# Kernel optimization log

Measured on AMD Instinct MI355X. Metric: run time of the kernel, lower is better.

Reference implementation:

```python
import jax, jax.numpy as jnp
import numpy as np

D = 2048
N_DRUG, N_PROT = 10000, 20000
E = 100000


def setup_inputs() -> dict:
    key = jax.random.key(0)
    ks = jax.random.split(key, 10)
    return {
        "x_drug": jax.random.normal(ks[0], (N_DRUG, D), dtype=jnp.float32),
        "x_protein": jax.random.normal(ks[1], (N_PROT, D), dtype=jnp.float32),
        "rel_ddi": jax.random.normal(ks[2], (D,), dtype=jnp.float32),
        "rel_dpi": jax.random.normal(ks[3], (D,), dtype=jnp.float32),
        "ddi_src": jax.random.randint(ks[4], (E,), 0, N_DRUG, dtype=jnp.int64 if jax.config.jax_enable_x64 else jnp.int32),
        "ddi_dst": jax.random.randint(ks[5], (E,), 0, N_DRUG, dtype=jnp.int64 if jax.config.jax_enable_x64 else jnp.int32),
        "dpi_src": jax.random.randint(ks[6], (E,), 0, N_DRUG, dtype=jnp.int64 if jax.config.jax_enable_x64 else jnp.int32),
        "dpi_dst": jax.random.randint(ks[7], (E,), 0, N_PROT, dtype=jnp.int64 if jax.config.jax_enable_x64 else jnp.int32),
        "ppi_src": jax.random.randint(ks[8], (E,), 0, N_PROT, dtype=jnp.int64 if jax.config.jax_enable_x64 else jnp.int32),
        "ppi_dst": jax.random.randint(ks[9], (E,), 0, N_PROT, dtype=jnp.int64 if jax.config.jax_enable_x64 else jnp.int32),
    }


def _edge_score(x_src, x_dst, src, dst, rel):
    # gather [E, D] head/tail, DistMult-style multiply-reduce, clamp to [0, 1]
    head = x_src[src]
    tail = x_dst[dst]
    score = jnp.sum(head * rel * tail, axis=-1)
    return jnp.clip(score, 0.0, 1.0)


def reference(x_drug, x_protein, rel_ddi, rel_dpi,
              ddi_src, ddi_dst, dpi_src, dpi_dst, ppi_src, ppi_dst):
    score_ddi = _edge_score(x_drug, x_drug, ddi_src, ddi_dst, rel_ddi)
    score_dpi = _edge_score(x_drug, x_protein, dpi_src, dpi_dst, rel_dpi)
    # NOTE: original module (faithfully) applies the DPI relation to PPI edges
    score_ppi = _edge_score(x_protein, x_protein, ppi_src, ppi_dst, rel_dpi)
    return (score_ddi, score_dpi, score_ppi)
```

## Files before the change

kernel.cpp:

```cpp
#include <hip/hip_runtime.h>
#include <hip/hip_fp16.h>

#define D4 512
#define T4 256
#define K_EDGES 16

__global__ __launch_bounds__(256) void cvt16(
    const float4* __restrict__ xd, const float4* __restrict__ xp,
    __half* __restrict__ drug16, __half* __restrict__ prot16,
    int nd4, int np4)
{
    int i = blockIdx.x * blockDim.x + threadIdx.x;
    const int total = nd4 + np4;
    for (; i < total; i += gridDim.x * blockDim.x) {
        float4 v; __half* o; int idx;
        if (i < nd4) { v = xd[i]; o = drug16; idx = i; }
        else         { v = xp[i - nd4]; o = prot16; idx = i - nd4; }
        __half2 h01 = __floats2half2_rn(v.x, v.y);
        __half2 h23 = __floats2half2_rn(v.z, v.w);
        uint2 pk = make_uint2(*(const unsigned*)&h01, *(const unsigned*)&h23);
        ((uint2*)o)[idx] = pk;
    }
}

__global__ void zero_ints(int* __restrict__ p, int n) {
    int i = blockIdx.x * blockDim.x + threadIdx.x;
    if (i < n) p[i] = 0;
}

__global__ void hist3(const int* __restrict__ s0, const int* __restrict__ s1,
                      const int* __restrict__ s2, int E,
                      int* __restrict__ cnt, int ndp) {
    int i = blockIdx.x * blockDim.x + threadIdx.x;
    const int total = 3 * E;
    for (; i < total; i += gridDim.x * blockDim.x) {
        if (i < E)           atomicAdd(&cnt[s0[i]], 1);
        else if (i < 2 * E)  atomicAdd(&cnt[ndp + s1[i - E]], 1);
        else                 atomicAdd(&cnt[2 * ndp + s2[i - 2 * E]], 1);
    }
}

__global__ void alloc3(const int* __restrict__ cnt, int* __restrict__ base,
                       int* __restrict__ cursors, int ndp, int CB) {
    int i = blockIdx.x * blockDim.x + threadIdx.x;
    if (i >= CB) return;
    const int lane = threadIdx.x & 63;
    const int g = (i < ndp) ? 0 : (i < 2 * ndp) ? 1 : 2;
    int c = cnt[i];
    int x = c;
#pragma unroll
    for (int d = 1; d < 64; d <<= 1) {
        int y = __shfl_up(x, d, 64);
        if (lane >= d) x += y;
    }
    int tot = __shfl(x, 63);
    int wb = 0;
    if (lane == 63) wb = atomicAdd(&cursors[g], tot);
    wb = __shfl(wb, 63);
    base[i] = wb + x - c;
}

__global__ void scatter3(const int* __restrict__ s0, const int* __restrict__ d0_,
                         const int* __restrict__ s1, const int* __restrict__ d1_,
                         const int* __restrict__ s2, const int* __restrict__ d2_,
                         int E, int* __restrict__ base, int ndp,
                         int* __restrict__ sorted, int* __restrict__ sd) {
    int i = blockIdx.x * blockDim.x + threadIdx.x;
    const int total = 3 * E;
    for (; i < total; i += gridDim.x * blockDim.x) {
        if (i < E) {
            int s = s0[i], d = d0_[i];
            int p = atomicAdd(&base[s], 1);
            sorted[p] = i; sd[p] = (s << 16) | d;
        } else if (i < 2 * E) {
            int k = i - E; int s = s1[k], d = d1_[k];
            int p = atomicAdd(&base[ndp + s], 1);
            sorted[E + p] = k; sd[E + p] = (s << 16) | d;
        } else {
            int k = i - 2 * E; int s = s2[k], d = d2_[k];
            int p = atomicAdd(&base[2 * ndp + s], 1);
            sorted[2 * E + p] = k; sd[2 * E + p] = (s << 16) | d;
        }
    }
}

__global__ __launch_bounds__(256) void score16(
    const float4* __restrict__ drug16, const float4* __restrict__ prot16,
    const float4* __restrict__ rddi,  const float4* __restrict__ rdpi,
    const int* __restrict__ sorted, const int* __restrict__ sd,
    int* __restrict__ refine, int* __restrict__ rcnt,
    float* __restrict__ out, int E)
{
    const int lane = threadIdx.x & 63;
    const int wpb = blockDim.x >> 6;
    const int wid = blockIdx.x * wpb + (threadIdx.x >> 6);
    const int nw = gridDim.x * wpb;
    const int cpr = (E + K_EDGES - 1) / K_EDGES;
    const int total_chunks = 3 * cpr;

    for (int c = wid; c < total_chunks; c += nw) {
        const int r = (c >= 2 * cpr) ? 2 : (c >= cpr) ? 1 : 0;
        const int ci = c - r * cpr;
        const int e_lo = ci * K_EDGES;
        const int n = min(K_EDGES, E - e_lo);

        const float4* xh = (r < 2) ? drug16 : prot16;
        const float4* xt = (r == 0) ? drug16 : prot16;
        const float4* rel = (r == 0) ? rddi : rdpi;
        const int* sl  = sorted + (size_t)r * E + e_lo;
        const int* sdl = sd     + (size_t)r * E + e_lo;
        float* o = out + (size_t)r * E;

        int eL = 0, sdL = 0;
        if (lane < n) { eL = sl[lane]; sdL = sdl[lane]; }

        float4 hr[8];
        int cur = -1;

        for (int i = 0; i < n; ++i) {
            const int sdi = __shfl(sdL, i);
            const int e   = __shfl(eL, i);
            const int s = sdi >> 16;
            if (s != cur) {
                cur = s;
                const float4* hp = xh + (size_t)s * T4;
#pragma unroll
                for (int g = 0; g < 4; ++g) {
                    float4 hv = hp[g * 64 + lane];
                    const __half2* h2 = (const __half2*)&hv;
                    float4 r0 = rel[2 * (g * 64 + lane)];
                    float4 r1 = rel[2 * (g * 64 + lane) + 1];
                    float2 f0 = __half22float2(h2[0]);
                    float2 f1 = __half22float2(h2[1]);
                    float2 f2 = __half22float2(h2[2]);
                    float2 f3 = __half22float2(h2[3]);
                    hr[2 * g].x     = f0.x * r0.x;
                    hr[2 * g].y     = f0.y * r0.y;
                    hr[2 * g].z     = f1.x * r0.z;
                    hr[2 * g].w     = f1.y * r0.w;
                    hr[2 * g + 1].x = f2.x * r1.x;
                    hr[2 * g + 1].y = f2.y * r1.y;
                    hr[2 * g + 1].z = f3.x * r1.z;
                    hr[2 * g + 1].w = f3.y * r1.w;
                }
            }
            const float4* tq = xt + (size_t)(sdi & 0xffff) * T4;
            float a0 = 0.f, a1 = 0.f, a2 = 0.f, a3 = 0.f;
#pragma unroll
            for (int g = 0; g < 4; ++g) {
                float4 tv = tq[g * 64 + lane];
                const __half2* t2 = (const __half2*)&tv;
                float2 f0 = __half22float2(t2[0]);
                float2 f1 = __half22float2(t2[1]);
                float2 f2 = __half22float2(t2[2]);
                float2 f3 = __half22float2(t2[3]);
                a0 = fmaf(hr[2 * g].x, f0.x, a0);
                a1 = fmaf(hr[2 * g].y, f0.y, a1);
                a2 = fmaf(hr[2 * g].z, f1.x, a2);
                a3 = fmaf(hr[2 * g].w, f1.y, a3);
                a0 = fmaf(hr[2 * g + 1].x, f2.x, a0);
                a1 = fmaf(hr[2 * g + 1].y, f2.y, a1);
                a2 = fmaf(hr[2 * g + 1].z, f3.x, a2);
                a3 = fmaf(hr[2 * g + 1].w, f3.y, a3);
            }
            float acc = (a0 + a1) + (a2 + a3);
#pragma unroll
            for (int off = 32; off; off >>= 1) acc += __shfl_down(acc, off, 64);
            if (lane == 0) {
                o[e] = fminf(fmaxf(acc, 0.f), 1.f);
                if (acc > -1.5f && acc < 2.5f) {
                    int p = atomicAdd(rcnt, 1);
                    refine[p] = (r << 20) | e;
                }
            }
        }
    }
}

__global__ __launch_bounds__(256) void refine_f32(
    const float4* __restrict__ xdrug, const float4* __restrict__ xprot,
    const float4* __restrict__ rddi,  const float4* __restrict__ rdpi,
    const int* __restrict__ ddi_src, const int* __restrict__ ddi_dst,
    const int* __restrict__ dpi_src, const int* __restrict__ dpi_dst,
    const int* __restrict__ ppi_src, const int* __restrict__ ppi_dst,
    const int* __restrict__ refine, const int* __restrict__ rcnt,
    float* __restrict__ out, int E)
{
    const int lane = threadIdx.x & 63;
    const int wpb = blockDim.x >> 6;
    const int wid = blockIdx.x * wpb + (threadIdx.x >> 6);
    const int nw = gridDim.x * wpb;
    const int count = rcnt[0];
    for (int k = wid; k < count; k += nw) {
        const int pe = refine[k];
        const int r = pe >> 20, e = pe & 0xFFFFF;
        const float4 *hp, *tp, *rel;
        if (r == 0)      { hp = xdrug + (size_t)ddi_src[e] * D4; tp = xdrug + (size_t)ddi_dst[e] * D4; rel = rddi; }
        else if (r == 1) { hp = xdrug + (size_t)dpi_src[e] * D4; tp = xprot + (size_t)dpi_dst[e] * D4; rel = rdpi; }
        else             { hp = xprot + (size_t)ppi_src[e] * D4; tp = xprot + (size_t)ppi_dst[e] * D4; rel = rdpi; }
        float a0 = 0.f, a1 = 0.f, a2 = 0.f, a3 = 0.f;
#pragma unroll
        for (int j = 0; j < 8; ++j) {
            const int idx = j * 64 + lane;
            float4 h = hp[idx], t = tp[idx], rv = rel[idx];
            a0 = fmaf(h.x * rv.x, t.x, a0);
            a1 = fmaf(h.y * rv.y, t.y, a1);
            a2 = fmaf(h.z * rv.z, t.z, a2);
            a3 = fmaf(h.w * rv.w, t.w, a3);
        }
        float acc = (a0 + a1) + (a2 + a3);
#pragma unroll
        for (int off = 32; off; off >>= 1) acc += __shfl_down(acc, off, 64);
        if (lane == 0) out[(size_t)r * E + e] = fminf(fmaxf(acc, 0.f), 1.f);
    }
}

__global__ __launch_bounds__(256) void score_f32(
    const float4* __restrict__ xdrug, const float4* __restrict__ xprot,
    const float4* __restrict__ rddi,  const float4* __restrict__ rdpi,
    const int* __restrict__ sorted, const int* __restrict__ sd,
    float* __restrict__ out, int E)
{
    const int lane = threadIdx.x & 63;
    const int wpb = blockDim.x >> 6;
    const int wid = blockIdx.x * wpb + (threadIdx.x >> 6);
    const int nw = gridDim.x * wpb;
    const int cpr = (E + K_EDGES - 1) / K_EDGES;
    const int total_chunks = 3 * cpr;

    for (int c = wid; c < total_chunks; c += nw) {
        const int r = (c >= 2 * cpr) ? 2 : (c >= cpr) ? 1 : 0;
        const int ci = c - r * cpr;
        const int e_lo = ci * K_EDGES;
        const int n = min(K_EDGES, E - e_lo);

        const float4 *xs, *xd, *rel;
        if (r == 0)      { xs = xdrug; xd = xdrug; rel = rddi; }
        else if (r == 1) { xs = xdrug; xd = xprot; rel = rdpi; }
        else             { xs = xprot; xd = xprot; rel = rdpi; }
        const int* sl  = sorted + (size_t)r * E + e_lo;
        const int* sdl = sd     + (size_t)r * E + e_lo;
        float* o = out + (size_t)r * E;

        float4 hr[8];
        int cur = -1;
        for (int i = 0; i < n; ++i) {
            const int e = sl[i];
            const int sdi = sdl[i];
            const int s = sdi >> 16;
            if (s != cur) {
                cur = s;
                const float4* hp = xs + (size_t)s * D4;
#pragma unroll
                for (int j = 0; j < 8; ++j) {
                    float4 h = hp[j * 64 + lane], rv = rel[j * 64 + lane];
                    hr[j].x = h.x * rv.x; hr[j].y = h.y * rv.y;
                    hr[j].z = h.z * rv.z; hr[j].w = h.w * rv.w;
                }
            }
            const float4* tp = xd + (size_t)(sdi & 0xffff) * D4;
            float acc = 0.f;
#pragma unroll
            for (int j = 0; j < 8; ++j) {
                float4 t = tp[j * 64 + lane];
                acc = fmaf(hr[j].x, t.x, acc);
                acc = fmaf(hr[j].y, t.y, acc);
                acc = fmaf(hr[j].z, t.z, acc);
                acc = fmaf(hr[j].w, t.w, acc);
            }
#pragma unroll
            for (int off = 32; off; off >>= 1) acc += __shfl_down(acc, off, 64);
            if (lane == 0) o[e] = fminf(fmaxf(acc, 0.f), 1.f);
        }
    }
}

__global__ __launch_bounds__(256) void edge_score_all(
    const float4* __restrict__ xdrug, const float4* __restrict__ xprot,
    const float4* __restrict__ rddi,  const float4* __restrict__ rdpi,
    const int* __restrict__ ddi_src, const int* __restrict__ ddi_dst,
    const int* __restrict__ dpi_src, const int* __restrict__ dpi_dst,
    const int* __restrict__ ppi_src, const int* __restrict__ ppi_dst,
    float* __restrict__ out, int E)
{
    __shared__ float4 srel[2][D4];
    for (int i = threadIdx.x; i < D4; i += blockDim.x) {
        srel[0][i] = rddi[i];
        srel[1][i] = rdpi[i];
    }
    __syncthreads();
    const int lane = threadIdx.x & 63;
    const int wpb = blockDim.x >> 6;
    int wid = blockIdx.x * wpb + (threadIdx.x >> 6);
    const int nw = gridDim.x * wpb;
    const int total = 3 * E;
    for (int e = wid; e < total; e += nw) {
        const float4 *hp, *tp;
        int sel;
        if (e < E)          { hp = xdrug + (size_t)ddi_src[e] * D4; tp = xdrug + (size_t)ddi_dst[e] * D4; sel = 0; }
        else if (e < 2 * E) { int k = e - E;     hp = xdrug + (size_t)dpi_src[k] * D4; tp = xprot + (size_t)dpi_dst[k] * D4; sel = 1; }
        else                { int k = e - 2 * E; hp = xprot + (size_t)ppi_src[k] * D4; tp = xprot + (size_t)ppi_dst[k] * D4; sel = 1; }
        float acc = 0.f;
#pragma unroll
        for (int j = 0; j < 8; ++j) {
            const int idx = j * 64 + lane;
            float4 h = hp[idx], t = tp[idx], rr = srel[sel][idx];
            acc = fmaf(h.x * rr.x, t.x, acc);
            acc = fmaf(h.y * rr.y, t.y, acc);
            acc = fmaf(h.z * rr.z, t.z, acc);
            acc = fmaf(h.w * rr.w, t.w, acc);
        }
#pragma unroll
        for (int off = 32; off; off >>= 1) acc += __shfl_down(acc, off, 64);
        if (lane == 0) out[e] = fminf(fmaxf(acc, 0.f), 1.f);
    }
}

extern "C" void kernel_launch(void* const* d_in, const int* in_sizes, int n_in,
                              void* d_out, int out_size, void* d_ws, size_t ws_size,
                              hipStream_t stream) {
    const float* x_drug    = (const float*)d_in[0];
    const float* x_protein = (const float*)d_in[1];
    const float* rel_ddi   = (const float*)d_in[2];
    const float* rel_dpi   = (const float*)d_in[3];
    const int* ddi_src = (const int*)d_in[4];
    const int* ddi_dst = (const int*)d_in[5];
    const int* dpi_src = (const int*)d_in[6];
    const int* dpi_dst = (const int*)d_in[7];
    const int* ppi_src = (const int*)d_in[8];
    const int* ppi_dst = (const int*)d_in[9];

    const int D  = in_sizes[2];
    const int nd = in_sizes[0] / D;
    const int np = in_sizes[1] / D;
    const int E  = in_sizes[4];
    float* out = (float*)d_out;

    const int ndp = ((nd + 63) / 64) * 64;
    const int npp = ((np + 63) / 64) * 64;
    const int CB  = 2 * ndp + npp;

    const size_t b_d16 = (size_t)nd * D * 2;
    const size_t b_p16 = (size_t)np * D * 2;
    const size_t ints_sort = (size_t)(2 * CB + 16 + 6 * E) * sizeof(int);
    const size_t need_sort = ints_sort;
    const size_t need_full = b_d16 + b_p16 + ints_sort + (size_t)3 * E * sizeof(int);

    if (ws_size < need_sort) {
        edge_score_all<<<2048, 256, 0, stream>>>(
            (const float4*)x_drug, (const float4*)x_protein,
            (const float4*)rel_ddi, (const float4*)rel_dpi,
            ddi_src, ddi_dst, dpi_src, dpi_dst, ppi_src, ppi_dst, out, E);
        return;
    }

    const bool full = (ws_size >= need_full);
    char* wp = (char*)d_ws;
    __half* drug16 = nullptr; __half* prot16 = nullptr;
    if (full) {
        drug16 = (__half*)wp;  wp += b_d16;
        prot16 = (__half*)wp;  wp += b_p16;
    }
    int* cnt    = (int*)wp;
    int* aux    = cnt + CB;
    int* base   = aux + 16;
    int* sorted = base + CB;
    int* sd     = sorted + 3 * E;
    int* refine = sd + 3 * E;

    if (full)
        cvt16<<<2048, 256, 0, stream>>>(
            (const float4*)x_drug, (const float4*)x_protein,
            drug16, prot16, nd * (D / 4), np * (D / 4));

    zero_ints<<<(CB + 16 + 255) / 256, 256, 0, stream>>>(cnt, CB + 16);
    hist3<<<1024, 256, 0, stream>>>(ddi_src, dpi_src, ppi_src, E, cnt, ndp);
    alloc3<<<(CB + 255) / 256, 256, 0, stream>>>(cnt, base, aux, ndp, CB);
    scatter3<<<1024, 256, 0, stream>>>(ddi_src, ddi_dst, dpi_src, dpi_dst,
                                       ppi_src, ppi_dst, E, base, ndp, sorted, sd);

    if (full) {
        score16<<<2048, 256, 0, stream>>>(
            (const float4*)drug16, (const float4*)prot16,
            (const float4*)rel_ddi, (const float4*)rel_dpi,
            sorted, sd, refine, aux + 8, out, E);
        refine_f32<<<1024, 256, 0, stream>>>(
            (const float4*)x_drug, (const float4*)x_protein,
            (const float4*)rel_ddi, (const float4*)rel_dpi,
            ddi_src, ddi_dst, dpi_src, dpi_dst, ppi_src, ppi_dst,
            refine, aux + 8, out, E);
    } else {
        score_f32<<<2048, 256, 0, stream>>>(
            (const float4*)x_drug, (const float4*)x_protein,
            (const float4*)rel_ddi, (const float4*)rel_dpi,
            sorted, sd, out, E);
    }
}
```

Before: 579.1 us.

## Fuse fp32 refinement into fp16 scoring kernel with dynamic chunk queue

The separate refine_f32 kernel and its global refine list are removed. Edges whose fp16 score lands near the clamp band are now recomputed in fp32 inline within score16, which also takes chunks from an atomic work queue. The zeroing kernel is folded into the fp16 conversion kernel. This saves two launches and the refine-list traffic, but puts divergent fp32 work inside the main loop and narrows the refine band, which slightly raises the accuracy risk.

Result: slower. 697.6 us (+20.5%).

```diff
diff --git a/kernel.cpp b/kernel.cpp
--- a/kernel.cpp
+++ b/kernel.cpp
@@ -4,15 +4,19 @@
 #define D4 512
 #define T4 256
 #define K_EDGES 16
-
-__global__ __launch_bounds__(256) void cvt16(
+#define BAND_LO (-1.0f)
+#define BAND_HI (2.0f)
+
+__global__ __launch_bounds__(256) void cvt_zero(
     const float4* __restrict__ xd, const float4* __restrict__ xp,
     __half* __restrict__ drug16, __half* __restrict__ prot16,
-    int nd4, int np4)
+    int nd4, int np4, int* __restrict__ zp, int zn)
 {
-    int i = blockIdx.x * blockDim.x + threadIdx.x;
+    const int stride = gridDim.x * blockDim.x;
+    int i = blockIdx.x * blockDim.x + threadIdx.x;
+    for (int k = i; k < zn; k += stride) zp[k] = 0;
     const int total = nd4 + np4;
-    for (; i < total; i += gridDim.x * blockDim.x) {
+    for (; i < total; i += stride) {
         float4 v; __half* o; int idx;
         if (i < nd4) { v = xd[i]; o = drug16; idx = i; }
         else         { v = xp[i - nd4]; o = prot16; idx = i - nd4; }
@@ -86,10 +90,10 @@
 
 __global__ __launch_bounds__(256) void score16(
     const float4* __restrict__ drug16, const float4* __restrict__ prot16,
+    const float4* __restrict__ xdrug, const float4* __restrict__ xprot,
     const float4* __restrict__ rddi,  const float4* __restrict__ rdpi,
     const int* __restrict__ sorted, const int* __restrict__ sd,
-    int* __restrict__ refine, int* __restrict__ rcnt,
-    float* __restrict__ out, int E)
+    int* __restrict__ queue, float* __restrict__ out, int E)
 {
     const int lane = threadIdx.x & 63;
     const int wpb = blockDim.x >> 6;
@@ -98,15 +102,18 @@
     const int cpr = (E + K_EDGES - 1) / K_EDGES;
     const int total_chunks = 3 * cpr;
 
-    for (int c = wid; c < total_chunks; c += nw) {
+    int c = wid;
+    while (c < total_chunks) {
         const int r = (c >= 2 * cpr) ? 2 : (c >= cpr) ? 1 : 0;
         const int ci = c - r * cpr;
         const int e_lo = ci * K_EDGES;
         const int n = min(K_EDGES, E - e_lo);
 
-        const float4* xh = (r < 2) ? drug16 : prot16;
-        const float4* xt = (r == 0) ? drug16 : prot16;
-        const float4* rel = (r == 0) ? rddi : rdpi;
+        const float4* xh   = (r < 2)  ? drug16 : prot16;
+        const float4* xt   = (r == 0) ? drug16 : prot16;
+        const float4* xh32 = (r < 2)  ? xdrug  : xprot;
+        const float4* xt32 = (r == 0) ? xdrug  : xprot;
+        const float4* rel  = (r == 0) ? rddi   : rdpi;
         const int* sl  = sorted + (size_t)r * E + e_lo;
         const int* sdl = sd     + (size_t)r * E + e_lo;
         float* o = out + (size_t)r * E;
@@ -121,6 +128,7 @@
             const int sdi = __shfl(sdL, i);
             const int e   = __shfl(eL, i);
             const int s = sdi >> 16;
+            const int d = sdi & 0xffff;
             if (s != cur) {
                 cur = s;
                 const float4* hp = xh + (size_t)s * T4;
@@ -144,7 +152,7 @@
                     hr[2 * g + 1].w = f3.y * r1.w;
                 }
             }
-            const float4* tq = xt + (size_t)(sdi & 0xffff) * T4;
+            const float4* tq = xt + (size_t)d * T4;
             float a0 = 0.f, a1 = 0.f, a2 = 0.f, a3 = 0.f;
 #pragma unroll
             for (int g = 0; g < 4; ++g) {
@@ -166,52 +174,33 @@
             float acc = (a0 + a1) + (a2 + a3);
 #pragma unroll
             for (int off = 32; off; off >>= 1) acc += __shfl_down(acc, off, 64);
-            if (lane == 0) {
-                o[e] = fminf(fmaxf(acc, 0.f), 1.f);
-                if (acc > -1.5f && acc < 2.5f) {
-                    int p = atomicAdd(rcnt, 1);
-                    refine[p] = (r << 20) | e;
+            const float accb = __shfl(acc, 0);
+
+            if (accb > BAND_LO && accb < BAND_HI) {
+                const float4* hp32 = xh32 + (size_t)s * D4;
+                const float4* tp32 = xt32 + (size_t)d * D4;
+                float b0 = 0.f, b1 = 0.f, b2 = 0.f, b3 = 0.f;
+#pragma unroll
+                for (int j = 0; j < 8; ++j) {
+                    const int idx = j * 64 + lane;
+                    float4 h = hp32[idx], t = tp32[idx], rv = rel[idx];
+                    b0 = fmaf(h.x * rv.x, t.x, b0);
+                    b1 = fmaf(h.y * rv.y, t.y, b1);
+                    b2 = fmaf(h.z * rv.z, t.z, b2);
+                    b3 = fmaf(h.w * rv.w, t.w, b3);
                 }
+                float bcc = (b0 + b1) + (b2 + b3);
+#pragma unroll
+                for (int off = 32; off; off >>= 1) bcc += __shfl_down(bcc, off, 64);
+                if (lane == 0) o[e] = fminf(fmaxf(bcc, 0.f), 1.f);
+            } else if (lane == 0) {
+                o[e] = fminf(fmaxf(accb, 0.f), 1.f);
             }
         }
-    }
-}
-
-__global__ __launch_bounds__(256) void refine_f32(
-    const float4* __restrict__ xdrug, const float4* __restrict__ xprot,
-    const float4* __restrict__ rddi,  const float4* __restrict__ rdpi,
-    const int* __restrict__ ddi_src, const int* __restrict__ ddi_dst,
-    const int* __restrict__ dpi_src, const int* __restrict__ dpi_dst,
-    const int* __restrict__ ppi_src, const int* __restrict__ ppi_dst,
-    const int* __restrict__ refine, const int* __restrict__ rcnt,
-    float* __restrict__ out, int E)
-{
-    const int lane = threadIdx.x & 63;
-    const int wpb = blockDim.x >> 6;
-    const int wid = blockIdx.x * wpb + (threadIdx.x >> 6);
-    const int nw = gridDim.x * wpb;
-    const int count = rcnt[0];
-    for (int k = wid; k < count; k += nw) {
-        const int pe = refine[k];
-        const int r = pe >> 20, e = pe & 0xFFFFF;
-        const float4 *hp, *tp, *rel;
-        if (r == 0)      { hp = xdrug + (size_t)ddi_src[e] * D4; tp = xdrug + (size_t)ddi_dst[e] * D4; rel = rddi; }
-        else if (r == 1) { hp = xdrug + (size_t)dpi_src[e] * D4; tp = xprot + (size_t)dpi_dst[e] * D4; rel = rdpi; }
-        else             { hp = xprot + (size_t)ppi_src[e] * D4; tp = xprot + (size_t)ppi_dst[e] * D4; rel = rdpi; }
-        float a0 = 0.f, a1 = 0.f, a2 = 0.f, a3 = 0.f;
-#pragma unroll
-        for (int j = 0; j < 8; ++j) {
-            const int idx = j * 64 + lane;
-            float4 h = hp[idx], t = tp[idx], rv = rel[idx];
-            a0 = fmaf(h.x * rv.x, t.x, a0);
-            a1 = fmaf(h.y * rv.y, t.y, a1);
-            a2 = fmaf(h.z * rv.z, t.z, a2);
-            a3 = fmaf(h.w * rv.w, t.w, a3);
-        }
-        float acc = (a0 + a1) + (a2 + a3);
-#pragma unroll
-        for (int off = 32; off; off >>= 1) acc += __shfl_down(acc, off, 64);
-        if (lane == 0) out[(size_t)r * E + e] = fminf(fmaxf(acc, 0.f), 1.f);
+
+        int nc = 0;
+        if (lane == 0) nc = atomicAdd(queue, 1);
+        c = nw + __shfl(nc, 0);
     }
 }
 
@@ -344,7 +333,7 @@
     const size_t b_p16 = (size_t)np * D * 2;
     const size_t ints_sort = (size_t)(2 * CB + 16 + 6 * E) * sizeof(int);
     const size_t need_sort = ints_sort;
-    const size_t need_full = b_d16 + b_p16 + ints_sort + (size_t)3 * E * sizeof(int);
+    const size_t need_full = b_d16 + b_p16 + ints_sort;
 
     if (ws_size < need_sort) {
         edge_score_all<<<2048, 256, 0, stream>>>(
@@ -366,14 +355,14 @@
     int* base   = aux + 16;
     int* sorted = base + CB;
     int* sd     = sorted + 3 * E;
-    int* refine = sd + 3 * E;
-
-    if (full)
-        cvt16<<<2048, 256, 0, stream>>>(
+
+    if (full) {
+        cvt_zero<<<2048, 256, 0, stream>>>(
             (const float4*)x_drug, (const float4*)x_protein,
-            drug16, prot16, nd * (D / 4), np * (D / 4));
-
-    zero_ints<<<(CB + 16 + 255) / 256, 256, 0, stream>>>(cnt, CB + 16);
+            drug16, prot16, nd * (D / 4), np * (D / 4), cnt, CB + 16);
+    } else {
+        zero_ints<<<(CB + 16 + 255) / 256, 256, 0, stream>>>(cnt, CB + 16);
+    }
     hist3<<<1024, 256, 0, stream>>>(ddi_src, dpi_src, ppi_src, E, cnt, ndp);
     alloc3<<<(CB + 255) / 256, 256, 0, stream>>>(cnt, base, aux, ndp, CB);
     scatter3<<<1024, 256, 0, stream>>>(ddi_src, ddi_dst, dpi_src, dpi_dst,
@@ -382,13 +371,9 @@
     if (full) {
         score16<<<2048, 256, 0, stream>>>(
             (const float4*)drug16, (const float4*)prot16,
-            (const float4*)rel_ddi, (const float4*)rel_dpi,
-            sorted, sd, refine, aux + 8, out, E);
-        refine_f32<<<1024, 256, 0, stream>>>(
             (const float4*)x_drug, (const float4*)x_protein,
             (const float4*)rel_ddi, (const float4*)rel_dpi,
-            ddi_src, ddi_dst, dpi_src, dpi_dst, ppi_src, ppi_dst,
-            refine, aux + 8, out, E);
+            sorted, sd, aux + 8, out, E);
     } else {
         score_f32<<<2048, 256, 0, stream>>>(
             (const float4*)x_drug, (const float4*)x_protein,
```
